# Performance work log

Hardware: AMD Instinct MI355X
Metric: run time of the kernel (lower is better)

Reference implementation:

```python
import jax, jax.numpy as jnp
import numpy as np

N0, N1, N2 = 60000, 15000, 3750
K, P = 32, 15
R0 = 0.5  # kernel extent at level 0; doubles per level (first_subsampling_dl*deform_radius scaled to unit-cube data)


def kpconv(q_pts, s_pts, neigh_idx, feats, kpoints, W, extent):
    """Rigid KPConv. q_pts [Nq,3], s_pts [Ns,3], neigh_idx [Nq,K] (shadow=Ns),
    feats [Ns,Cin], kpoints [P,3] unit-scale, W [P,Cin,Cout]."""
    s_pts_p = jnp.concatenate([s_pts, jnp.full((1, 3), 1e6, s_pts.dtype)], 0)
    feats_p = jnp.concatenate([feats, jnp.zeros((1, feats.shape[1]), feats.dtype)], 0)
    neigh_pts = s_pts_p[neigh_idx]                       # [Nq,K,3] gather
    neigh_f = feats_p[neigh_idx]                         # [Nq,K,Cin] gather
    diff = neigh_pts - q_pts[:, None, :]                 # [Nq,K,3]
    dist = jnp.sqrt(jnp.sum((diff[:, :, None, :] - kpoints[None, None] * extent) ** 2, -1))
    infl = jnp.maximum(0.0, 1.0 - dist / extent)         # [Nq,K,P] linear influence
    fk = jnp.einsum('nkp,nkc->npc', infl, neigh_f)       # per-kernel-point aggregation
    out = jnp.einsum('npc,pco->no', fk, W)
    return jax.nn.leaky_relu(out, 0.1)


def detection_scores(neighbor, features):
    # verbatim translation of KPFCNN.detection_scores (eval mode)
    n_total = features.shape[0]
    feats = jnp.concatenate([features, jnp.zeros_like(features[:1])], 0)
    neighbor = jnp.concatenate([neighbor, jnp.full_like(neighbor[:1], n_total)], 0)
    feats = feats / (jnp.max(feats) + 1e-6)
    nf = feats[neighbor]                                 # [N+1,K,C]
    nnum = jnp.maximum(jnp.sum(jnp.sum(nf, -1) != 0, -1, keepdims=True), 1)
    mean_f = jnp.sum(nf, 1) / nnum
    local_max_score = jax.nn.softplus(feats - mean_f)
    depth_max = jnp.max(feats, 1, keepdims=True)
    all_scores = local_max_score * (feats / (1e-6 + depth_max))
    scores = jnp.max(all_scores, 1, keepdims=True)
    detected = jnp.max((feats == jnp.max(nf, 1)).astype(feats.dtype), 1, keepdims=True)
    return (scores * detected)[:-1]


def reference(features, points0, points1, points2, neighbors0, neighbors1, neighbors2,
              pools0, pools1, upsamples0, upsamples1, kpoints, W1, W2, W3, W4, W5, Wu1, Wu2):
    # ---- encoder ----
    f = kpconv(points0, points0, neighbors0, features, kpoints, W1, R0)      # simple         [N0,64]
    skip0 = f
    f = kpconv(points1, points0, pools0, f, kpoints, W2, R0)                 # simple_strided [N1,64]
    f = kpconv(points1, points1, neighbors1, f, kpoints, W3, 2 * R0)         # simple         [N1,128]
    skip1 = f
    f = kpconv(points2, points1, pools1, f, kpoints, W4, 2 * R0)             # simple_strided [N2,128]
    f = kpconv(points2, points2, neighbors2, f, kpoints, W5, 4 * R0)         # simple         [N2,256]
    # ---- decoder: nearest_upsample + skip concat + unary ----
    f = jnp.concatenate([f[upsamples1[:, 0]], skip1], 1)                     # [N1,384] (1.5*256)
    f = jax.nn.leaky_relu(f @ Wu1, 0.1)                                      # unary          [N1,128]
    f = jnp.concatenate([f[upsamples0[:, 0]], skip0], 1)                     # [N0,192]
    f = f @ Wu2                                                              # last_unary     [N0,32]
    scores = detection_scores(neighbors0, f)
    fnorm = f / jnp.maximum(jnp.linalg.norm(f, axis=-1, keepdims=True), 1e-12)
    return fnorm, scores


def setup_inputs() -> dict:
    key = jax.random.key(0)
    ks = jax.random.split(key, 20)
    inp = {
        'features': jax.random.normal(ks[0], (N0, 1), jnp.float32),
        'points0': jax.random.uniform(ks[1], (N0, 3), jnp.float32),
        'points1': jax.random.uniform(ks[2], (N1, 3), jnp.float32),
        'points2': jax.random.uniform(ks[3], (N2, 3), jnp.float32),
        'neighbors0': jax.random.randint(ks[4], (N0, K), 0, N0, jnp.int32),
        'neighbors1': jax.random.randint(ks[5], (N1, K), 0, N1, jnp.int32),
        'neighbors2': jax.random.randint(ks[6], (N2, K), 0, N2, jnp.int32),
        'pools0': jax.random.randint(ks[7], (N1, K), 0, N0, jnp.int32),
        'pools1': jax.random.randint(ks[8], (N2, K), 0, N1, jnp.int32),
        'upsamples0': jax.random.randint(ks[9], (N0, 1), 0, N1, jnp.int32),
        'upsamples1': jax.random.randint(ks[10], (N1, 1), 0, N2, jnp.int32),
        'kpoints': jax.random.normal(ks[11], (P, 3), jnp.float32) * 0.5,
    }
    def w(k, shape, fan_in):
        return jax.random.normal(k, shape, jnp.float32) / np.sqrt(fan_in)
    inp['W1'] = w(ks[12], (P, 1, 64), P * 1)
    inp['W2'] = w(ks[13], (P, 64, 64), P * 64)
    inp['W3'] = w(ks[14], (P, 64, 128), P * 64)
    inp['W4'] = w(ks[15], (P, 128, 128), P * 128)
    inp['W5'] = w(ks[16], (P, 128, 256), P * 128)
    inp['Wu1'] = w(ks[17], (384, 128), 384)
    inp['Wu2'] = w(ks[18], (192, 32), 192)
    return inp
```

## Files before the change

kernel.cpp:

```cpp
#include <hip/hip_runtime.h>
#include <math.h>

static const int cN0 = 60000;
static const int cN1 = 15000;
static const int cN2 = 3750;

typedef __bf16 bf16x8 __attribute__((ext_vector_type(8)));
typedef float f32x4 __attribute__((ext_vector_type(4)));

#define GLOAD_LDS16(gsrc, ldst)                                                        \
  __builtin_amdgcn_global_load_lds((const __attribute__((address_space(1))) void*)(gsrc), \
                                   (__attribute__((address_space(3))) void*)(ldst), 16, 0, 0)

__global__ __launch_bounds__(256) void prep_kernel(
    const float* __restrict__ pts0, const float* __restrict__ feat,
    const float* __restrict__ pts1, const float* __restrict__ pts2,
    const float* __restrict__ W2, const float* __restrict__ W3, const float* __restrict__ W4,
    const float* __restrict__ W5, const float* __restrict__ Wu1, const float* __restrict__ Wu2,
    float4* __restrict__ pk0, float4* __restrict__ pk1, float4* __restrict__ pk2,
    __bf16* __restrict__ T2, __bf16* __restrict__ T3, __bf16* __restrict__ T4,
    __bf16* __restrict__ T5, __bf16* __restrict__ Tu1, __bf16* __restrict__ Tu2) {
  int role = blockIdx.y;
  int tid = blockIdx.x * 256 + threadIdx.x;
  int stride = gridDim.x * 256;
  if (role < 3) {
    const float* p = role == 0 ? pts0 : (role == 1 ? pts1 : pts2);
    float4* o = role == 0 ? pk0 : (role == 1 ? pk1 : pk2);
    int n = role == 0 ? cN0 : (role == 1 ? cN1 : cN2);
    for (int i = tid; i < n; i += stride) {
      float4 v;
      v.x = p[(size_t)i * 3 + 0];
      v.y = p[(size_t)i * 3 + 1];
      v.z = p[(size_t)i * 3 + 2];
      v.w = role == 0 ? feat[i] : 0.f;
      o[i] = v;
    }
  } else {
    const float* src;
    __bf16* dst;
    int Kd, Nd;
    switch (role) {
      case 3: src = W2;  dst = T2;  Kd = 960;  Nd = 64;  break;
      case 4: src = W3;  dst = T3;  Kd = 960;  Nd = 128; break;
      case 5: src = W4;  dst = T4;  Kd = 1920; Nd = 128; break;
      case 6: src = W5;  dst = T5;  Kd = 1920; Nd = 256; break;
      case 7: src = Wu1; dst = Tu1; Kd = 384;  Nd = 128; break;
      default: src = Wu2; dst = Tu2; Kd = 192; Nd = 32;  break;
    }
    int total = Kd * Nd;
    for (int e = tid; e < total; e += stride) {
      int n = e / Kd, k = e % Kd;
      dst[e] = (__bf16)src[(size_t)k * Nd + n];
    }
  }
}

__global__ __launch_bounds__(256) void kpconv_l1(
    const float4* __restrict__ pk, const int* __restrict__ neigh,
    const float* __restrict__ kpts, const float* __restrict__ W1,
    __bf16* __restrict__ f0, float extent) {
  const int t = threadIdx.x;
  const int n0b = blockIdx.x * 16;
  __shared__ float s_nb[32][16][4];
  __shared__ float s_fk[16][16];
  __shared__ float s_W[960];
  for (int i = t; i < 960; i += 256) s_W[i] = W1[i];
  #pragma unroll
  for (int i = 0; i < 2; ++i) {
    int e = t + i * 256;
    int pt = e & 15, k = e >> 4;
    int idx = neigh[(size_t)(n0b + pt) * 32 + k];
    *(float4*)&s_nb[k][pt][0] = pk[idx];
  }
  __syncthreads();
  const int lane = t & 63, wave = t >> 6;
  const int g = lane >> 4, p_raw = lane & 15;
  const int p = p_raw < 15 ? p_raw : 0;
  const int pt = wave * 4 + g;
  const int n = n0b + pt;
  const float inv = 1.f / extent;
  float4 q = pk[n];
  const float kx = q.x + kpts[p * 3 + 0] * extent;
  const float ky = q.y + kpts[p * 3 + 1] * extent;
  const float kz = q.z + kpts[p * 3 + 2] * extent;
  float fk = 0.f;
  #pragma unroll 8
  for (int k = 0; k < 32; ++k) {
    f32x4 rec = *(const f32x4*)&s_nb[k][pt][0];
    float dx = rec[0] - kx, dy = rec[1] - ky, dz = rec[2] - kz;
    float d = sqrtf(dx * dx + dy * dy + dz * dz);
    fk += fmaxf(0.f, 1.f - d * inv) * rec[3];
  }
  if (p_raw < 15) s_fk[pt][p_raw] = fk;
  __syncthreads();
  #pragma unroll
  for (int o = 0; o < 4; ++o) {
    int e = o * 256 + t;
    int opt = e >> 6, c = e & 63;
    float acc = 0.f;
    #pragma unroll
    for (int pp = 0; pp < 15; ++pp) acc += s_fk[opt][pp] * s_W[pp * 64 + c];
    acc = acc > 0.f ? acc : 0.1f * acc;
    f0[(size_t)(n0b + opt) * 64 + c] = (__bf16)acc;
  }
}

template <int CIN, int COUT, int BM, bool BDBUF>
__global__ __launch_bounds__(512) void kpconv_fused(
    const float4* __restrict__ qp, const float4* __restrict__ sp,
    const int* __restrict__ neigh, const __bf16* __restrict__ F,
    const float* __restrict__ kpts, const __bf16* __restrict__ BT,
    __bf16* __restrict__ out, int M, float extent) {
  constexpr int KK = 15 * CIN;
  constexpr int KT = KK / 64;
  constexpr int CPRow = CIN / 8;
  constexpr int RPB = 8192 / CIN;
  constexpr int GS = RPB / 2;
  constexpr int BP = RPB / 32;
  constexpr int NB = BM * 32 / RPB;
  constexpr int WPP = 8 / BP;
  constexpr int FBUF = 8192;
  constexpr int RG = BM / 16;
  constexpr int CG = 8 / RG;
  constexpr int NJ = COUT / (16 * CG);
  constexpr int SMEM_FK = BM * KK * 2;
  constexpr int SMEM = SMEM_FK + BP * 1280 + BM * 16 + 2 * FBUF * 2;

  __shared__ __align__(16) char smem[SMEM];
  __bf16* s_fk   = (__bf16*)smem;
  __bf16* s_infl = (__bf16*)(smem + SMEM_FK);
  float4* s_q    = (float4*)(smem + SMEM_FK + BP * 1280);
  __bf16* s_F    = (__bf16*)(smem + SMEM_FK + BP * 1280 + BM * 16);
  __bf16* s_B    = s_F;

  const int t = threadIdx.x;
  const int w = t >> 6, l = t & 63;
  const int c16 = l & 15, g4 = l >> 4;
  const int m0 = blockIdx.x * BM;
  const int* nb_base = neigh + (size_t)m0 * 32;
  int rlim = (M - m0) * 32 - 1;
  if (rlim > BM * 32 - 1) rlim = BM * 32 - 1;

  const int gb = t / CPRow;
  const int ch = t % CPRow;
  int idxg[NB][2];
  #pragma unroll
  for (int b = 0; b < NB; ++b)
    #pragma unroll
    for (int j = 0; j < 2; ++j) {
      int r = b * RPB + gb + j * GS;
      idxg[b][j] = nb_base[r < rlim ? r : rlim];
    }
  const int ii  = t & 1;
  const int pq4 = ((t >> 1) & 3) * 4;
  const int row_i = gb + ii * GS;
  const int pt_i = row_i >> 5, kk_i = row_i & 31;
  const float inv = 1.f / extent;
  float kpx[4], kpy[4], kpz[4];
  #pragma unroll
  for (int pi = 0; pi < 4; ++pi) {
    int p = pq4 + pi; if (p > 14) p = 14;
    kpx[pi] = kpts[p * 3 + 0] * extent;
    kpy[pi] = kpts[p * 3 + 1] * extent;
    kpz[pi] = kpts[p * 3 + 2] * extent;
  }
  if (t < BM) { int n = m0 + t; s_q[t] = qp[n < M ? n : M - 1]; }

  auto stageF = [&](int buf, const int (&ig)[2]) {
    #pragma unroll
    for (int j = 0; j < 2; ++j) {
      int k = (gb + j * GS) & 31;
      const __bf16* src = F + (size_t)ig[j] * CIN + (ch ^ ((k >> 3) & 3)) * 8;
      GLOAD_LDS16(src, s_F + buf * FBUF + (j * 512 + t) * 8);
    }
  };
  auto inflC = [&](const float4& spv, int b, float (&v)[4]) {
    float4 q = s_q[b * BP + pt_i];
    float sx = spv.x - q.x, sy = spv.y - q.y, sz = spv.z - q.z;
    #pragma unroll
    for (int pi = 0; pi < 4; ++pi) {
      float dx = sx - kpx[pi], dy = sy - kpy[pi], dz = sz - kpz[pi];
      float d = sqrtf(dx * dx + dy * dy + dz * dz);
      v[pi] = fmaxf(0.f, 1.f - d * inv);
    }
  };
  auto inflStore = [&](const float (&v)[4]) {
    #pragma unroll
    for (int pi = 0; pi < 4; ++pi) {
      int p = pq4 + pi;
      if (p < 15) s_infl[pt_i * 640 + p * 40 + kk_i] = (__bf16)v[pi];
    }
  };
  auto mfmaBatch = [&](int b, int buf) {
    const int pt_loc = w / WPP;
    const int cc0 = (w % WPP) * 2;
    const __bf16* Fb = s_F + buf * FBUF + pt_loc * (32 * CIN);
    bf16x8 a = *(const bf16x8*)&s_infl[pt_loc * 640 + c16 * 40 + g4 * 8];
    const int row = b * BP + pt_loc;
    #pragma unroll
    for (int ci = 0; ci < 2; ++ci) {
      const int cc = cc0 + ci;
      const int Lc = cc * 2 + (c16 >> 3);
      const int pc = Lc ^ g4;
      bf16x8 bv;
      #pragma unroll
      for (int j = 0; j < 8; ++j)
        bv[j] = Fb[(g4 * 8 + j) * CIN + pc * 8 + (c16 & 7)];
      f32x4 acc = __builtin_amdgcn_mfma_f32_16x16x32_bf16(a, bv, (f32x4){0.f, 0.f, 0.f, 0.f}, 0, 0, 0);
      #pragma unroll
      for (int r = 0; r < 4; ++r) {
        int p = g4 * 4 + r;
        if (p < 15) {
          int Lf = p * CPRow + Lc;
          int phys = (Lf & ~7) | ((Lf & 7) ^ (row & 7));
          s_fk[(size_t)row * KK + phys * 8 + (c16 & 7)] = (__bf16)acc[r];
        }
      }
    }
  };

  asm volatile("s_waitcnt lgkmcnt(0)" ::: "memory");
  __builtin_amdgcn_s_barrier();
  __builtin_amdgcn_sched_barrier(0);

  float4 spc, spn;
  {
    float4 sp0 = sp[idxg[0][ii]];
    stageF(0, idxg[0]);
    spc = sp[idxg[NB > 1 ? 1 : 0][ii]];
    float v0[4];
    inflC(sp0, 0, v0);
    inflStore(v0);
  }
  __builtin_amdgcn_sched_barrier(0);
  #pragma unroll
  for (int b = 0; b < NB; ++b) {
    if (b + 1 < NB) stageF((b + 1) & 1, idxg[b + 1]);
    if (b + 2 < NB) spn = sp[idxg[b + 2][ii]];
    float vn[4];
    if (b + 1 < NB) inflC(spc, b + 1, vn);
    if (b + 1 < NB) { asm volatile("s_waitcnt vmcnt(3)" ::: "memory"); }
    else            { asm volatile("s_waitcnt vmcnt(0)" ::: "memory"); }
    asm volatile("s_waitcnt lgkmcnt(0)" ::: "memory");
    __builtin_amdgcn_s_barrier();
    __builtin_amdgcn_sched_barrier(0);
    mfmaBatch(b, b & 1);
    asm volatile("s_waitcnt lgkmcnt(0)" ::: "memory");
    __builtin_amdgcn_s_barrier();
    __builtin_amdgcn_sched_barrier(0);
    if (b + 1 < NB) { inflStore(vn); spc = spn; }
  }
  __syncthreads();

  const int wr = w / CG, wc = w % CG;
  f32x4 acc[NJ];
  #pragma unroll
  for (int j = 0; j < NJ; ++j) acc[j] = (f32x4){0.f, 0.f, 0.f, 0.f};
  auto stageB = [&](int buf, int kt) {
    #pragma unroll
    for (int rnd = 0; rnd < COUT / 64; ++rnd) {
      int slot = rnd * 512 + t;
      int row = slot >> 3, bch = slot & 7;
      GLOAD_LDS16(BT + (size_t)row * KK + kt * 64 + (bch ^ (row & 7)) * 8,
                  s_B + buf * (COUT * 64) + slot * 8);
    }
  };
  const __bf16* fkrow = s_fk + (size_t)(wr * 16 + c16) * KK;
  auto computeTile = [&](int kt, int buf) {
    bf16x8 af[2];
    #pragma unroll
    for (int s = 0; s < 2; ++s)
      af[s] = *(const bf16x8*)&fkrow[((kt * 8 + (s * 4 + g4)) & ~7 | (((s * 4 + g4) & 7) ^ (c16 & 7))) * 8 + (kt * 8 & ~7) * 0];
    #pragma unroll
    for (int s = 0; s < 2; ++s)
      af[s] = *(const bf16x8*)&fkrow[(kt * 8 + ((s * 4 + g4) ^ (c16 & 7))) * 8];
    const __bf16* Bb = s_B + buf * (COUT * 64);
    #pragma unroll
    for (int j = 0; j < NJ; ++j) {
      int n = wc * (16 * NJ) + j * 16 + c16;
      #pragma unroll
      for (int s = 0; s < 2; ++s) {
        bf16x8 bf = *(const bf16x8*)&Bb[n * 64 + ((s * 4 + g4) ^ (n & 7)) * 8];
        acc[j] = __builtin_amdgcn_mfma_f32_16x16x32_bf16(af[s], bf, acc[j], 0, 0, 0);
      }
    }
  };
  if (BDBUF) {
    stageB(0, 0);
    __syncthreads();
    for (int kt = 0; kt < KT; ++kt) {
      if (kt + 1 < KT) stageB((kt + 1) & 1, kt + 1);
      computeTile(kt, kt & 1);
      __syncthreads();
    }
  } else {
    for (int kt = 0; kt < KT; ++kt) {
      stageB(0, kt);
      __syncthreads();
      computeTile(kt, 0);
      __syncthreads();
    }
  }
  #pragma unroll
  for (int j = 0; j < NJ; ++j)
    #pragma unroll
    for (int r = 0; r < 4; ++r) {
      int row = m0 + wr * 16 + g4 * 4 + r;
      int col = wc * (16 * NJ) + j * 16 + c16;
      if (row < M) {
        float v = acc[j][r];
        v = v > 0.f ? v : 0.1f * v;
        out[(size_t)row * COUT + col] = (__bf16)v;
      }
    }
}

template <bool LEAKY, bool GATHER, bool OUTF32, bool MAXOUT>
__global__ __launch_bounds__(256, 2) void gemm_mfma(
    const __bf16* __restrict__ A1, const __bf16* __restrict__ A2,
    const int* __restrict__ gidx, const int K1,
    const __bf16* __restrict__ BT, void* __restrict__ Cout,
    const int M, const int N, const int KK, unsigned* __restrict__ gmax) {
  __shared__ __bf16 sA[2][4096];
  __shared__ __bf16 sB[2][4096];
  __shared__ float s_max[4];
  const int t = threadIdx.x;
  const int lane = t & 63, wave = t >> 6;
  const int wr = wave >> 1, wc = wave & 1;
  const int m0 = blockIdx.y * 64, n0 = blockIdx.x * 64;
  const int K2 = KK - K1;

  const __bf16* a1row[2];
  const __bf16* a2row[2];
  const __bf16* brow_[2];
  int csrc[2], wbase[2];
  #pragma unroll
  for (int r = 0; r < 2; ++r) {
    int slot = r * 256 + wave * 64 + lane;
    int row = slot >> 3;
    csrc[r] = ((slot & 7) ^ (row & 7)) * 8;
    wbase[r] = (r * 256 + wave * 64) * 8;
    int gm = m0 + row; if (gm > M - 1) gm = M - 1;
    if (GATHER) {
      a1row[r] = A1 + (size_t)gidx[gm] * K1;
      a2row[r] = A2 + (size_t)gm * (size_t)K2;
    } else {
      a1row[r] = A1 + (size_t)gm * (size_t)KK;
    }
    int gn = n0 + row; if (gn > N - 1) gn = N - 1;
    brow_[r] = BT + (size_t)gn * (size_t)KK;
  }

  int offA[2][2], offB[2][2];
  #pragma unroll
  for (int i = 0; i < 2; ++i)
    #pragma unroll
    for (int s = 0; s < 2; ++s) {
      int ra = wr * 32 + i * 16 + (lane & 15);
      int rb = wc * 32 + i * 16 + (lane & 15);
      int chn = s * 4 + (lane >> 4);
      offA[i][s] = ra * 64 + (chn ^ (ra & 7)) * 8;
      offB[i][s] = rb * 64 + (chn ^ (rb & 7)) * 8;
    }

  f32x4 acc[2][2];
  #pragma unroll
  for (int i = 0; i < 2; ++i)
    #pragma unroll
    for (int j = 0; j < 2; ++j) acc[i][j] = (f32x4){0.f, 0.f, 0.f, 0.f};

  auto stage = [&](int buf, int k0) {
    #pragma unroll
    for (int r = 0; r < 2; ++r) {
      int kg = k0 + csrc[r];
      const __bf16* asrc;
      if (GATHER) asrc = (kg < K1) ? (a1row[r] + kg) : (a2row[r] + (kg - K1));
      else        asrc = a1row[r] + kg;
      GLOAD_LDS16(asrc, &sA[buf][wbase[r]]);
      GLOAD_LDS16(brow_[r] + kg, &sB[buf][wbase[r]]);
    }
  };

  stage(0, 0);
  __syncthreads();
  const int nk = KK >> 6;
  int cur = 0;
  for (int kt = 0; kt < nk; ++kt) {
    if (kt + 1 < nk) stage(cur ^ 1, (kt + 1) << 6);
    #pragma unroll
    for (int s = 0; s < 2; ++s) {
      bf16x8 a0 = *(const bf16x8*)&sA[cur][offA[0][s]];
      bf16x8 a1 = *(const bf16x8*)&sA[cur][offA[1][s]];
      bf16x8 b0 = *(const bf16x8*)&sB[cur][offB[0][s]];
      bf16x8 b1 = *(const bf16x8*)&sB[cur][offB[1][s]];
      acc[0][0] = __builtin_amdgcn_mfma_f32_16x16x32_bf16(a0, b0, acc[0][0], 0, 0, 0);
      acc[0][1] = __builtin_amdgcn_mfma_f32_16x16x32_bf16(a0, b1, acc[0][1], 0, 0, 0);
      acc[1][0] = __builtin_amdgcn_mfma_f32_16x16x32_bf16(a1, b0, acc[1][0], 0, 0, 0);
      acc[1][1] = __builtin_amdgcn_mfma_f32_16x16x32_bf16(a1, b1, acc[1][1], 0, 0, 0);
    }
    __syncthreads();
    cur ^= 1;
  }

  float lmax = 0.f;
  #pragma unroll
  for (int i = 0; i < 2; ++i)
    #pragma unroll
    for (int j = 0; j < 2; ++j)
      #pragma unroll
      for (int g = 0; g < 4; ++g) {
        int row = m0 + wr * 32 + i * 16 + (lane >> 4) * 4 + g;
        int col = n0 + wc * 32 + j * 16 + (lane & 15);
        if (row < M && col < N) {
          float v = acc[i][j][g];
          if (LEAKY) v = v > 0.f ? v : 0.1f * v;
          if (MAXOUT) lmax = fmaxf(lmax, v);
          if (OUTF32) ((float*)Cout)[(size_t)row * N + col] = v;
          else        ((__bf16*)Cout)[(size_t)row * N + col] = (__bf16)v;
        }
      }
  if (MAXOUT) {
    #pragma unroll
    for (int s = 32; s >= 1; s >>= 1) lmax = fmaxf(lmax, __shfl_xor(lmax, s, 64));
    if (lane == 0) s_max[wave] = lmax;
    __syncthreads();
    if (t == 0) {
      float mm = fmaxf(fmaxf(s_max[0], s_max[1]), fmaxf(s_max[2], s_max[3]));
      atomicMax(gmax, __float_as_uint(mm));
    }
  }
}

__global__ __launch_bounds__(256) void detect_kernel(
    const float* __restrict__ f6, const int* __restrict__ neigh,
    const float* __restrict__ gm_ptr, float* __restrict__ out_fnorm,
    float* __restrict__ out_scores, int N) {
  int n = blockIdx.x * 8 + (threadIdx.x >> 5);
  int c = threadIdx.x & 31;
  if (n >= N) return;
  float denom = gm_ptr[0] + 1e-6f;
  float fown = f6[(size_t)n * 32 + c];
  int idx_l = neigh[(size_t)n * 32 + c];
  float colsum = 0.f, colmax = -1e30f;
  for (int k = 0; k < 32; ++k) {
    int idx = __shfl(idx_l, k, 32);
    float v = f6[(size_t)idx * 32 + c];
    colsum += v;
    colmax = fmaxf(colmax, v);
  }
  float fs = fown / denom;
  float mean = (colsum / denom) * (1.f / 32.f);
  float x = fs - mean;
  float lms = fmaxf(x, 0.f) + log1pf(expf(-fabsf(x)));
  float dm = fs;
  #pragma unroll
  for (int s = 16; s >= 1; s >>= 1) dm = fmaxf(dm, __shfl_xor(dm, s, 32));
  float as = lms * fs / (1e-6f + dm);
  float sc = as;
  #pragma unroll
  for (int s = 16; s >= 1; s >>= 1) sc = fmaxf(sc, __shfl_xor(sc, s, 32));
  float det = (fown == colmax) ? 1.f : 0.f;
  #pragma unroll
  for (int s = 16; s >= 1; s >>= 1) det = fmaxf(det, __shfl_xor(det, s, 32));
  float nn2 = fown * fown;
  #pragma unroll
  for (int s = 16; s >= 1; s >>= 1) nn2 += __shfl_xor(nn2, s, 32);
  float inv_nrm = 1.f / fmaxf(sqrtf(nn2), 1e-12f);
  out_fnorm[(size_t)n * 32 + c] = fown * inv_nrm;
  if (c == 0) out_scores[n] = sc * det;
}

extern "C" void kernel_launch(void* const* d_in, const int* in_sizes, int n_in,
                              void* d_out, int out_size, void* d_ws, size_t ws_size,
                              hipStream_t stream) {
  const float* features  = (const float*)d_in[0];
  const float* points0   = (const float*)d_in[1];
  const float* points1   = (const float*)d_in[2];
  const float* points2   = (const float*)d_in[3];
  const int* neighbors0  = (const int*)d_in[4];
  const int* neighbors1  = (const int*)d_in[5];
  const int* neighbors2  = (const int*)d_in[6];
  const int* pools0      = (const int*)d_in[7];
  const int* pools1      = (const int*)d_in[8];
  const int* upsamples0  = (const int*)d_in[9];
  const int* upsamples1  = (const int*)d_in[10];
  const float* kpoints   = (const float*)d_in[11];
  const float* W1  = (const float*)d_in[12];
  const float* W2  = (const float*)d_in[13];
  const float* W3  = (const float*)d_in[14];
  const float* W4  = (const float*)d_in[15];
  const float* W5  = (const float*)d_in[16];
  const float* Wu1 = (const float*)d_in[17];
  const float* Wu2 = (const float*)d_in[18];

  const float R0 = 0.5f;

  char* wp = (char*)d_ws;
  auto alloc = [&](size_t bytes) {
    char* r = wp;
    wp += (bytes + 255) & ~(size_t)255;
    return r;
  };
  __bf16* f0b  = (__bf16*)alloc((size_t)cN0 * 64 * 2);
  __bf16* f1b  = (__bf16*)alloc((size_t)cN1 * 64 * 2);
  __bf16* f2b  = (__bf16*)alloc((size_t)cN1 * 128 * 2);
  __bf16* f3b  = (__bf16*)alloc((size_t)cN2 * 128 * 2);
  __bf16* f4b  = (__bf16*)alloc((size_t)cN2 * 256 * 2);
  __bf16* f5b  = (__bf16*)alloc((size_t)cN1 * 128 * 2);
  float*  f6   = (float*)alloc((size_t)cN0 * 32 * 4);
  __bf16* WT2  = (__bf16*)alloc(960 * 64 * 2);
  __bf16* WT3  = (__bf16*)alloc(960 * 128 * 2);
  __bf16* WT4  = (__bf16*)alloc(1920 * 128 * 2);
  __bf16* WT5  = (__bf16*)alloc(1920 * 256 * 2);
  __bf16* WTu1 = (__bf16*)alloc(384 * 128 * 2);
  __bf16* WTu2 = (__bf16*)alloc(192 * 32 * 2);
  unsigned* gm = (unsigned*)alloc(256);
  float4* pk0  = (float4*)alloc((size_t)cN0 * 16);
  float4* pk1  = (float4*)alloc((size_t)cN1 * 16);
  float4* pk2  = (float4*)alloc((size_t)cN2 * 16);

  prep_kernel<<<dim3(240, 9), 256, 0, stream>>>(
      points0, features, points1, points2, W2, W3, W4, W5, Wu1, Wu2,
      pk0, pk1, pk2, WT2, WT3, WT4, WT5, WTu1, WTu2);
  kpconv_l1<<<cN0 / 16, 256, 0, stream>>>(pk0, neighbors0, kpoints, W1, f0b, R0);

  kpconv_fused<64, 64, 64, true><<<(cN1 + 63) / 64, 512, 0, stream>>>(
      pk1, pk0, pools0, f0b, kpoints, WT2, f1b, cN1, R0);
  kpconv_fused<64, 128, 64, true><<<(cN1 + 63) / 64, 512, 0, stream>>>(
      pk1, pk1, neighbors1, f1b, kpoints, WT3, f2b, cN1, 2.f * R0);
  kpconv_fused<128, 128, 16, true><<<(cN2 + 15) / 16, 512, 0, stream>>>(
      pk2, pk1, pools1, f2b, kpoints, WT4, f3b, cN2, 2.f * R0);
  kpconv_fused<128, 256, 16, false><<<(cN2 + 15) / 16, 512, 0, stream>>>(
      pk2, pk2, neighbors2, f3b, kpoints, WT5, f4b, cN2, 4.f * R0);

  gemm_mfma<true, true, false, false><<<dim3(2, 235), 256, 0, stream>>>(
      f4b, f2b, upsamples1, 256, WTu1, f5b, cN1, 128, 384, nullptr);
  hipMemsetAsync(gm, 0, 4, stream);
  gemm_mfma<false, true, true, true><<<dim3(1, 938), 256, 0, stream>>>(
      f5b, f0b, upsamples0, 128, WTu2, f6, cN0, 32, 192, gm);

  float* out_fnorm = (float*)d_out;
  float* out_scores = out_fnorm + (size_t)cN0 * 32;
  detect_kernel<<<(cN0 + 7) / 8, 256, 0, stream>>>(f6, neighbors0, (const float*)gm,
                                                   out_fnorm, out_scores, cN0);
}
```

Baseline: 219.1 us.

## Retile kpconv gather batches, shrink level-1 blocks, add dedicated final GEMM kernel

Reorganizes the fused KPConv gather stage to use fixed 64-row batches, with per-thread influence indices loaded separately and wait counts adjusted to match. The level-1 convolutions drop from 64 to 32 query points per block, giving more blocks, and one of them switches off double-buffering. The final upsample GEMM (N=32, K=192) moves to a specialized d2_kernel that loads the full K slice into LDS at once and fuses the global max. The generic GEMM loses its unused output and max template paths. The aim is better occupancy and parallelism on the smaller layers, at the cost of less reuse per block.

New measurement: 205.1 us. 6.4% less time.

```diff
diff --git a/kernel.cpp b/kernel.cpp
--- a/kernel.cpp
+++ b/kernel.cpp
@@ -114,23 +114,22 @@
   constexpr int KK = 15 * CIN;
   constexpr int KT = KK / 64;
   constexpr int CPRow = CIN / 8;
-  constexpr int RPB = 8192 / CIN;
-  constexpr int GS = RPB / 2;
-  constexpr int BP = RPB / 32;
-  constexpr int NB = BM * 32 / RPB;
-  constexpr int WPP = 8 / BP;
-  constexpr int FBUF = 8192;
+  constexpr int G = CIN / 64;
+  constexpr int GS = 64 / G;
+  constexpr int NB = BM / 2;
+  constexpr int CPW = CIN / 64;
+  constexpr int FBUF = 64 * CIN;
   constexpr int RG = BM / 16;
   constexpr int CG = 8 / RG;
   constexpr int NJ = COUT / (16 * CG);
   constexpr int SMEM_FK = BM * KK * 2;
-  constexpr int SMEM = SMEM_FK + BP * 1280 + BM * 16 + 2 * FBUF * 2;
+  constexpr int SMEM = SMEM_FK + 2 * 1280 + BM * 16 + 2 * FBUF * 2;
 
   __shared__ __align__(16) char smem[SMEM];
   __bf16* s_fk   = (__bf16*)smem;
   __bf16* s_infl = (__bf16*)(smem + SMEM_FK);
-  float4* s_q    = (float4*)(smem + SMEM_FK + BP * 1280);
-  __bf16* s_F    = (__bf16*)(smem + SMEM_FK + BP * 1280 + BM * 16);
+  float4* s_q    = (float4*)(smem + SMEM_FK + 2 * 1280);
+  __bf16* s_F    = (__bf16*)(smem + SMEM_FK + 2 * 1280 + BM * 16);
   __bf16* s_B    = s_F;
 
   const int t = threadIdx.x;
@@ -143,18 +142,23 @@
 
   const int gb = t / CPRow;
   const int ch = t % CPRow;
-  int idxg[NB][2];
+  int idxg[NB][G];
   #pragma unroll
   for (int b = 0; b < NB; ++b)
     #pragma unroll
-    for (int j = 0; j < 2; ++j) {
-      int r = b * RPB + gb + j * GS;
+    for (int j = 0; j < G; ++j) {
+      int r = b * 64 + gb + j * GS;
       idxg[b][j] = nb_base[r < rlim ? r : rlim];
     }
-  const int ii  = t & 1;
-  const int pq4 = ((t >> 1) & 3) * 4;
-  const int row_i = gb + ii * GS;
+  const int row_i = (t >> 2) & 63;
+  const int pq4 = (t & 3) * 4;
   const int pt_i = row_i >> 5, kk_i = row_i & 31;
+  int idxi[NB];
+  #pragma unroll
+  for (int b = 0; b < NB; ++b) {
+    int r = b * 64 + row_i;
+    idxi[b] = nb_base[r < rlim ? r : rlim];
+  }
   const float inv = 1.f / extent;
   float kpx[4], kpy[4], kpz[4];
   #pragma unroll
@@ -166,16 +170,16 @@
   }
   if (t < BM) { int n = m0 + t; s_q[t] = qp[n < M ? n : M - 1]; }
 
-  auto stageF = [&](int buf, const int (&ig)[2]) {
-    #pragma unroll
-    for (int j = 0; j < 2; ++j) {
+  auto stageF = [&](int buf, const int (&ig)[G]) {
+    #pragma unroll
+    for (int j = 0; j < G; ++j) {
       int k = (gb + j * GS) & 31;
       const __bf16* src = F + (size_t)ig[j] * CIN + (ch ^ ((k >> 3) & 3)) * 8;
       GLOAD_LDS16(src, s_F + buf * FBUF + (j * 512 + t) * 8);
     }
   };
   auto inflC = [&](const float4& spv, int b, float (&v)[4]) {
-    float4 q = s_q[b * BP + pt_i];
+    float4 q = s_q[b * 2 + pt_i];
     float sx = spv.x - q.x, sy = spv.y - q.y, sz = spv.z - q.z;
     #pragma unroll
     for (int pi = 0; pi < 4; ++pi) {
@@ -185,20 +189,22 @@
     }
   };
   auto inflStore = [&](const float (&v)[4]) {
-    #pragma unroll
-    for (int pi = 0; pi < 4; ++pi) {
-      int p = pq4 + pi;
-      if (p < 15) s_infl[pt_i * 640 + p * 40 + kk_i] = (__bf16)v[pi];
+    if (t < 256) {
+      #pragma unroll
+      for (int pi = 0; pi < 4; ++pi) {
+        int p = pq4 + pi;
+        if (p < 15) s_infl[pt_i * 640 + p * 40 + kk_i] = (__bf16)v[pi];
+      }
     }
   };
   auto mfmaBatch = [&](int b, int buf) {
-    const int pt_loc = w / WPP;
-    const int cc0 = (w % WPP) * 2;
+    const int pt_loc = w / 4;
+    const int cc0 = (w & 3) * CPW;
     const __bf16* Fb = s_F + buf * FBUF + pt_loc * (32 * CIN);
     bf16x8 a = *(const bf16x8*)&s_infl[pt_loc * 640 + c16 * 40 + g4 * 8];
-    const int row = b * BP + pt_loc;
-    #pragma unroll
-    for (int ci = 0; ci < 2; ++ci) {
+    const int row = b * 2 + pt_loc;
+    #pragma unroll
+    for (int ci = 0; ci < CPW; ++ci) {
       const int cc = cc0 + ci;
       const int Lc = cc * 2 + (c16 >> 3);
       const int pc = Lc ^ g4;
@@ -225,9 +231,9 @@
 
   float4 spc, spn;
   {
-    float4 sp0 = sp[idxg[0][ii]];
     stageF(0, idxg[0]);
-    spc = sp[idxg[NB > 1 ? 1 : 0][ii]];
+    float4 sp0 = sp[idxi[0]];
+    spc = sp[idxi[1 < NB ? 1 : 0]];
     float v0[4];
     inflC(sp0, 0, v0);
     inflStore(v0);
@@ -236,11 +242,14 @@
   #pragma unroll
   for (int b = 0; b < NB; ++b) {
     if (b + 1 < NB) stageF((b + 1) & 1, idxg[b + 1]);
-    if (b + 2 < NB) spn = sp[idxg[b + 2][ii]];
+    if (b + 2 < NB) spn = sp[idxi[b + 2]];
     float vn[4];
     if (b + 1 < NB) inflC(spc, b + 1, vn);
-    if (b + 1 < NB) { asm volatile("s_waitcnt vmcnt(3)" ::: "memory"); }
-    else            { asm volatile("s_waitcnt vmcnt(0)" ::: "memory"); }
+    if (b == NB - 1)      { asm volatile("s_waitcnt vmcnt(0)" ::: "memory"); }
+    else if (b == NB - 2) { if (G == 1) asm volatile("s_waitcnt vmcnt(1)" ::: "memory");
+                            else        asm volatile("s_waitcnt vmcnt(2)" ::: "memory"); }
+    else                  { if (G == 1) asm volatile("s_waitcnt vmcnt(2)" ::: "memory");
+                            else        asm volatile("s_waitcnt vmcnt(3)" ::: "memory"); }
     asm volatile("s_waitcnt lgkmcnt(0)" ::: "memory");
     __builtin_amdgcn_s_barrier();
     __builtin_amdgcn_sched_barrier(0);
@@ -270,9 +279,6 @@
     bf16x8 af[2];
     #pragma unroll
     for (int s = 0; s < 2; ++s)
-      af[s] = *(const bf16x8*)&fkrow[((kt * 8 + (s * 4 + g4)) & ~7 | (((s * 4 + g4) & 7) ^ (c16 & 7))) * 8 + (kt * 8 & ~7) * 0];
-    #pragma unroll
-    for (int s = 0; s < 2; ++s)
       af[s] = *(const bf16x8*)&fkrow[(kt * 8 + ((s * 4 + g4) ^ (c16 & 7))) * 8];
     const __bf16* Bb = s_B + buf * (COUT * 64);
     #pragma unroll
@@ -315,15 +321,14 @@
     }
 }
 
-template <bool LEAKY, bool GATHER, bool OUTF32, bool MAXOUT>
+template <bool LEAKY, bool GATHER>
 __global__ __launch_bounds__(256, 2) void gemm_mfma(
     const __bf16* __restrict__ A1, const __bf16* __restrict__ A2,
     const int* __restrict__ gidx, const int K1,
-    const __bf16* __restrict__ BT, void* __restrict__ Cout,
-    const int M, const int N, const int KK, unsigned* __restrict__ gmax) {
+    const __bf16* __restrict__ BT, __bf16* __restrict__ Cout,
+    const int M, const int N, const int KK) {
   __shared__ __bf16 sA[2][4096];
   __shared__ __bf16 sB[2][4096];
-  __shared__ float s_max[4];
   const int t = threadIdx.x;
   const int lane = t & 63, wave = t >> 6;
   const int wr = wave >> 1, wc = wave & 1;
@@ -402,7 +407,6 @@
     cur ^= 1;
   }
 
-  float lmax = 0.f;
   #pragma unroll
   for (int i = 0; i < 2; ++i)
     #pragma unroll
@@ -414,20 +418,93 @@
         if (row < M && col < N) {
           float v = acc[i][j][g];
           if (LEAKY) v = v > 0.f ? v : 0.1f * v;
-          if (MAXOUT) lmax = fmaxf(lmax, v);
-          if (OUTF32) ((float*)Cout)[(size_t)row * N + col] = v;
-          else        ((__bf16*)Cout)[(size_t)row * N + col] = (__bf16)v;
+          Cout[(size_t)row * N + col] = (__bf16)v;
         }
       }
-  if (MAXOUT) {
-    #pragma unroll
-    for (int s = 32; s >= 1; s >>= 1) lmax = fmaxf(lmax, __shfl_xor(lmax, s, 64));
-    if (lane == 0) s_max[wave] = lmax;
-    __syncthreads();
-    if (t == 0) {
-      float mm = fmaxf(fmaxf(s_max[0], s_max[1]), fmaxf(s_max[2], s_max[3]));
-      atomicMax(gmax, __float_as_uint(mm));
-    }
+}
+
+__global__ __launch_bounds__(256) void d2_kernel(
+    const __bf16* __restrict__ f5b, const __bf16* __restrict__ f0b,
+    const int* __restrict__ up0, const __bf16* __restrict__ BT,
+    float* __restrict__ f6, int M, unsigned* __restrict__ gmax) {
+  __shared__ __bf16 sA[128 * 192];
+  __shared__ __bf16 sB[32 * 192];
+  __shared__ int s_g[128];
+  __shared__ float s_max[4];
+  const int t = threadIdx.x;
+  const int m0 = blockIdx.x * 128;
+  if (t < 128) { int m = m0 + t; s_g[t] = up0[m < M ? m : M - 1]; }
+  __syncthreads();
+  #pragma unroll
+  for (int rnd = 0; rnd < 3; ++rnd) {
+    int slot = rnd * 256 + t;
+    int row = slot / 24, chd = slot % 24;
+    int chs = (chd & ~7) | ((chd & 7) ^ (row & 7));
+    GLOAD_LDS16(BT + (size_t)row * 192 + chs * 8, sB + slot * 8);
+  }
+  #pragma unroll
+  for (int rnd = 0; rnd < 12; ++rnd) {
+    int slot = rnd * 256 + t;
+    int row = slot / 24, chd = slot % 24;
+    int chs = (chd & ~7) | ((chd & 7) ^ (row & 7));
+    int m = m0 + row; if (m > M - 1) m = M - 1;
+    const __bf16* src = (chs < 16) ? (f5b + (size_t)s_g[row] * 128 + chs * 8)
+                                   : (f0b + (size_t)m * 64 + (chs - 16) * 8);
+    GLOAD_LDS16(src, sA + slot * 8);
+  }
+  __syncthreads();
+  const int w = t >> 6, lane = t & 63;
+  const int c16 = lane & 15, g4 = lane >> 4;
+  f32x4 acc[2][2];
+  #pragma unroll
+  for (int i = 0; i < 2; ++i)
+    #pragma unroll
+    for (int j = 0; j < 2; ++j) acc[i][j] = (f32x4){0.f, 0.f, 0.f, 0.f};
+  #pragma unroll
+  for (int ks = 0; ks < 6; ++ks) {
+    bf16x8 a[2], b[2];
+    #pragma unroll
+    for (int i = 0; i < 2; ++i) {
+      int row = w * 32 + i * 16 + c16;
+      int chunk = ks * 4 + g4;
+      int phys = (chunk & ~7) | ((chunk & 7) ^ (row & 7));
+      a[i] = *(const bf16x8*)&sA[(row * 24 + phys) * 8];
+    }
+    #pragma unroll
+    for (int j = 0; j < 2; ++j) {
+      int n = j * 16 + c16;
+      int chunk = ks * 4 + g4;
+      int phys = (chunk & ~7) | ((chunk & 7) ^ (n & 7));
+      b[j] = *(const bf16x8*)&sB[(n * 24 + phys) * 8];
+    }
+    #pragma unroll
+    for (int i = 0; i < 2; ++i)
+      #pragma unroll
+      for (int j = 0; j < 2; ++j)
+        acc[i][j] = __builtin_amdgcn_mfma_f32_16x16x32_bf16(a[i], b[j], acc[i][j], 0, 0, 0);
+  }
+  float lmax = 0.f;
+  #pragma unroll
+  for (int i = 0; i < 2; ++i)
+    #pragma unroll
+    for (int j = 0; j < 2; ++j)
+      #pragma unroll
+      for (int g = 0; g < 4; ++g) {
+        int row = m0 + w * 32 + i * 16 + g4 * 4 + g;
+        int col = j * 16 + c16;
+        if (row < M) {
+          float v = acc[i][j][g];
+          lmax = fmaxf(lmax, v);
+          f6[(size_t)row * 32 + col] = v;
+        }
+      }
+  #pragma unroll
+  for (int s = 32; s >= 1; s >>= 1) lmax = fmaxf(lmax, __shfl_xor(lmax, s, 64));
+  if (lane == 0) s_max[w] = lmax;
+  __syncthreads();
+  if (t == 0) {
+    float mm = fmaxf(fmaxf(s_max[0], s_max[1]), fmaxf(s_max[2], s_max[3]));
+    atomicMax(gmax, __float_as_uint(mm));
   }
 }
 
@@ -524,20 +601,20 @@
       pk0, pk1, pk2, WT2, WT3, WT4, WT5, WTu1, WTu2);
   kpconv_l1<<<cN0 / 16, 256, 0, stream>>>(pk0, neighbors0, kpoints, W1, f0b, R0);
 
-  kpconv_fused<64, 64, 64, true><<<(cN1 + 63) / 64, 512, 0, stream>>>(
+  kpconv_fused<64, 64, 32, true><<<(cN1 + 31) / 32, 512, 0, stream>>>(
       pk1, pk0, pools0, f0b, kpoints, WT2, f1b, cN1, R0);
-  kpconv_fused<64, 128, 64, true><<<(cN1 + 63) / 64, 512, 0, stream>>>(
+  kpconv_fused<64, 128, 32, false><<<(cN1 + 31) / 32, 512, 0, stream>>>(
       pk1, pk1, neighbors1, f1b, kpoints, WT3, f2b, cN1, 2.f * R0);
   kpconv_fused<128, 128, 16, true><<<(cN2 + 15) / 16, 512, 0, stream>>>(
       pk2, pk1, pools1, f2b, kpoints, WT4, f3b, cN2, 2.f * R0);
   kpconv_fused<128, 256, 16, false><<<(cN2 + 15) / 16, 512, 0, stream>>>(
       pk2, pk2, neighbors2, f3b, kpoints, WT5, f4b, cN2, 4.f * R0);
 
-  gemm_mfma<true, true, false, false><<<dim3(2, 235), 256, 0, stream>>>(
-      f4b, f2b, upsamples1, 256, WTu1, f5b, cN1, 128, 384, nullptr);
+  gemm_mfma<true, true><<<dim3(2, 235), 256, 0, stream>>>(
+      f4b, f2b, upsamples1, 256, WTu1, f5b, cN1, 128, 384);
   hipMemsetAsync(gm, 0, 4, stream);
-  gemm_mfma<false, true, true, true><<<dim3(1, 938), 256, 0, stream>>>(
-      f5b, f0b, upsamples0, 128, WTu2, f6, cN0, 32, 192, gm);
+  d2_kernel<<<(cN0 + 127) / 128, 256, 0, stream>>>(
+      f5b, f0b, upsamples0, WTu2, f6, cN0, gm);
 
   float* out_fnorm = (float*)d_out;
   float* out_scores = out_fnorm + (size_t)cN0 * 32;
```
